# Kernel tuning notes

Hardware: AMD Instinct MI355X
Metric: run time of the kernel (lower is better)

## Reference

```python
import jax, jax.numpy as jnp
import numpy as np

N = 100000   # nodes
E = 1600000  # edges
D = 128      # input feature dim
H = 128      # hidden dim
L = 3        # gnn layers
G = 64       # graphs in batch
C = 2        # classes


def setup_inputs() -> dict:
    key = jax.random.key(0)
    ks = jax.random.split(key, 12)
    s = 0.05
    x = jax.random.normal(ks[0], (N, D), jnp.float32)
    edge_index = jax.random.randint(ks[1], (2, E), 0, N, dtype=jnp.int32)
    batch = jnp.sort(jax.random.randint(ks[2], (N,), 0, G, dtype=jnp.int32))
    return {
        "x": x,
        "edge_index": edge_index,
        "batch": batch,
        "W0": jax.random.normal(ks[3], (D, H), jnp.float32) * s,
        "b0": jnp.zeros((H,), jnp.float32),
        "Wg": jax.random.normal(ks[4], (L, H, H), jnp.float32) * s,
        "bg": jnp.zeros((L, H), jnp.float32),
        "Wc1": jax.random.normal(ks[5], (H, H), jnp.float32) * s,
        "bc1": jnp.zeros((H,), jnp.float32),
        "Wc2": jax.random.normal(ks[6], (H, C), jnp.float32) * s,
        "bc2": jnp.zeros((C,), jnp.float32),
    }


def reference(x, edge_index, batch, W0, b0, Wg, bg, Wc1, bc1, Wc2, bc2):
    # --- GCN normalization with self-loops (PyG gcn_norm) ---
    src, dst = edge_index[0], edge_index[1]
    loops = jnp.arange(N, dtype=src.dtype)
    src_f = jnp.concatenate([src, loops])  # [E+N] message sources (x_j)
    dst_f = jnp.concatenate([dst, loops])  # [E+N] aggregation targets
    deg = jax.ops.segment_sum(jnp.ones((E + N,), x.dtype), dst_f, num_segments=N)
    dinv = jnp.where(deg > 0, jax.lax.rsqrt(deg), 0.0)
    norm = (dinv[src_f] * dinv[dst_f])[:, None]  # [E+N, 1]

    # --- input linear + relu (dropout is identity in eval mode) ---
    h = jax.nn.relu(x @ W0 + b0)  # [N, H]

    # --- stacked GCNConv layers with residual + relu ---
    for l in range(L):
        xw = h @ Wg[l]  # [N, H]
        agg = jax.ops.segment_sum(xw[src_f] * norm, dst_f, num_segments=N) + bg[l]
        h = jax.nn.relu(h + agg)

    # --- global add pool over graphs ---
    pooled = jax.ops.segment_sum(h, batch, num_segments=G)  # [G, H]

    # --- classifier MLP + softmax ---
    z = jax.nn.relu(pooled @ Wc1 + bc1)
    return jax.nn.softmax(z @ Wc2 + bc2, axis=-1)  # [G, C]
```

## Files before the change

kernel.cpp:

```cpp
#include <hip/hip_runtime.h>

#define NN 100000
#define NE 1600000
#define HD 128
#define NG 64
#define NL 3
#define NBK 391
#define NEB 391
#define CAP 4608
#define NRB 6250
#define FP4_SCALE 8.0f
#define FP4_INV   0.125f

typedef __attribute__((ext_vector_type(8))) short bf16x8;
typedef __attribute__((ext_vector_type(4))) float f32x4;
typedef __attribute__((ext_vector_type(2))) float f32x2;
union U4 { uint4 u; bf16x8 b; };


__device__ __forceinline__ unsigned f2bf(float f) {
    unsigned u = __float_as_uint(f);
    return (u + 0x7FFFu + ((u >> 16) & 1u)) >> 16;
}
__device__ __forceinline__ float bf_lo(unsigned w) { return __uint_as_float(w << 16); }
__device__ __forceinline__ float bf_hi(unsigned w) { return __uint_as_float(w & 0xFFFF0000u); }
__device__ __forceinline__ unsigned cvt_pk_bf16(float lo, float hi) {
    unsigned r;
    asm("v_cvt_pk_bf16_f32 %0, %1, %2" : "=v"(r) : "v"(lo), "v"(hi));
    return r;
}


__global__ __launch_bounds__(256) void k_wconv(const float* __restrict__ W0,
                                               const float* __restrict__ Wg,
                                               unsigned* __restrict__ Wb) {
    int gid = blockIdx.x * 256 + threadIdx.x;
    for (int i = gid; i < 4 * 8192; i += 32 * 256) {
        int m = i >> 13;
        int r = i & 8191;
        int col = r & 127;
        int p = r >> 7;
        int k0, k1;
        if (m == 0) { k0 = 2 * p; k1 = 2 * p + 1; }
        else        { k0 = p;     k1 = p + 64;    }
        const float* Ws = (m == 0) ? W0 : (Wg + (m - 1) * 16384);
        float w0 = Ws[k0 * 128 + col];
        float w1 = Ws[k1 * 128 + col];
        Wb[m * 8192 + col * 64 + (((2 * p) ^ ((col & 7) << 3)) >> 1)] = (f2bf(w1) << 16) | f2bf(w0);
    }
}


__global__ __launch_bounds__(256) void k_bscatter(const int* __restrict__ src, const int* __restrict__ dst,
                                                  int* __restrict__ gcur, unsigned* __restrict__ pairs) {
    __shared__ int cnt[NBK];
    __shared__ int bse[NBK];
    __shared__ int rnk[NBK];
    for (int i = threadIdx.x; i < NBK; i += 256) { cnt[i] = 0; rnk[i] = 0; }
    __syncthreads();
    int base = blockIdx.x * 4096;
    int d[16];
#pragma unroll
    for (int j = 0; j < 16; j++) {
        int e = base + j * 256 + threadIdx.x;
        d[j] = (e < NE) ? dst[e] : -1;
        if (d[j] >= 0) atomicAdd(&cnt[((unsigned)d[j]) >> 8], 1);
    }
    __syncthreads();
    for (int i = threadIdx.x; i < NBK; i += 256) {
        int c = cnt[i];
        bse[i] = c ? atomicAdd(&gcur[i], c) : 0;
    }
    __syncthreads();
#pragma unroll
    for (int j = 0; j < 16; j++) {
        int e = base + j * 256 + threadIdx.x;
        if (e < NE) {
            int b = ((unsigned)d[j]) >> 8;
            int r = atomicAdd(&rnk[b], 1);
            int pos = bse[b] + r;
            if (pos < CAP)
                pairs[(size_t)b * CAP + pos] = (unsigned)src[e] | (((unsigned)d[j] & 255u) << 17);
        }
    }
}

__global__ __launch_bounds__(256) void k_bfill(const unsigned* __restrict__ pairs,
                                               const int* __restrict__ gcur,
                                               int* __restrict__ row_ptr, int* __restrict__ degA,
                                               float* __restrict__ dinv, unsigned* __restrict__ csr) {
    __shared__ int cnt[256];
    __shared__ int sm[256];
    __shared__ int cur[256];
    int t = threadIdx.x, k = blockIdx.x;
    int base = k * CAP;
    int ne = min(gcur[k], CAP);
    cnt[t] = 0;
    __syncthreads();
    for (int e = t; e < ne; e += 256) atomicAdd(&cnt[pairs[base + e] >> 17], 1);
    __syncthreads();
    int v = cnt[t];
    sm[t] = v;
    __syncthreads();
    for (int off = 1; off < 256; off <<= 1) {
        int add = (t >= off) ? sm[t - off] : 0;
        __syncthreads();
        sm[t] += add;
        __syncthreads();
    }
    int excl = base + sm[t] - v;
    int node = (k << 8) + t;
    if (node < NN) {
        row_ptr[node] = excl;
        degA[node] = v;
        dinv[node] = rsqrtf((float)(v + 1));
    }
    cur[t] = excl;
    __syncthreads();
    for (int e = t; e < ne; e += 256) {
        unsigned p = pairs[base + e];
        int pos = atomicAdd(&cur[p >> 17], 1);
        csr[pos] = (p & 0x1FFFFu) << 6;
    }
}


template <int MODE>
__global__ __launch_bounds__(256) void k_mgemm(
    const float* __restrict__ Xf, const unsigned* __restrict__ Xb,
    const unsigned* __restrict__ Wb, const float* __restrict__ bias,
    const float* __restrict__ dinv, unsigned* __restrict__ Out) {
    __shared__ unsigned short Bt[128 * 128];
    {
        const uint4* s4 = (const uint4*)Wb;
        uint4* d4 = (uint4*)Bt;
        for (int i = threadIdx.x; i < 2048; i += 256) d4[i] = s4[i];
    }
    __syncthreads();

    int lane = threadIdx.x & 63;
    int l15 = lane & 15, q = lane >> 4;
    int rb = blockIdx.x * 4 + (threadIdx.x >> 6);
    if (rb >= NRB) return;
    int r0 = rb * 16;

    U4 a[4];
    if (MODE == 0) {
        const float* xrow = Xf + (size_t)(r0 + l15) * 128 + q * 8;
#pragma unroll
        for (int kk = 0; kk < 4; kk++) {
            float4 f0 = *(const float4*)(xrow + kk * 32);
            float4 f1 = *(const float4*)(xrow + kk * 32 + 4);
            a[kk].u.x = (f2bf(f0.y) << 16) | f2bf(f0.x);
            a[kk].u.y = (f2bf(f0.w) << 16) | f2bf(f0.z);
            a[kk].u.z = (f2bf(f1.y) << 16) | f2bf(f1.x);
            a[kk].u.w = (f2bf(f1.w) << 16) | f2bf(f1.z);
        }
    } else {
        const unsigned* xrow = Xb + (size_t)(r0 + l15) * 64 + q * 4;
#pragma unroll
        for (int kk = 0; kk < 4; kk++) a[kk].u = *(const uint4*)(xrow + kk * 16);
    }

    f32x4 acc[8];
#pragma unroll
    for (int ct = 0; ct < 8; ct++) acc[ct] = (f32x4){0.f, 0.f, 0.f, 0.f};
#pragma unroll
    for (int kk = 0; kk < 4; kk++) {
#pragma unroll
        for (int ct = 0; ct < 8; ct++) {
            int col = ct * 16 + l15;
            int off = col * 128 + ((kk * 32 + q * 8) ^ ((col & 7) << 3));
            U4 b;
            b.u = *(const uint4*)&Bt[off];
            acc[ct] = __builtin_amdgcn_mfma_f32_16x16x32_bf16(a[kk].b, b.b, acc[ct], 0, 0, 0);
        }
    }

    if (MODE == 0) {
        float bv[8];
#pragma unroll
        for (int ct = 0; ct < 8; ct++) bv[ct] = bias[ct * 16 + l15];
#pragma unroll
        for (int r = 0; r < 4; r++) {
            int row = r0 + q * 4 + r;
#pragma unroll
            for (int ct = 0; ct < 4; ct++) {
                float lo = fmaxf(acc[ct][r] + bv[ct], 0.f);
                float hi = fmaxf(acc[ct + 4][r] + bv[ct + 4], 0.f);
                Out[(size_t)row * 64 + ct * 16 + l15] = cvt_pk_bf16(lo, hi);
            }
        }
    } else {
#pragma unroll
        for (int r = 0; r < 4; r++) {
            int row = r0 + q * 4 + r;
            float sc = dinv[row] * FP4_SCALE;
            unsigned dw = __builtin_amdgcn_cvt_scalef32_pk_fp4_f32(0u, acc[0][r] * sc, acc[4][r] * sc, 1.0f, 0);
            dw = __builtin_amdgcn_cvt_scalef32_pk_fp4_f32(dw, acc[2][r] * sc, acc[6][r] * sc, 1.0f, 1);
            dw = __builtin_amdgcn_cvt_scalef32_pk_fp4_f32(dw, acc[1][r] * sc, acc[5][r] * sc, 1.0f, 2);
            dw = __builtin_amdgcn_cvt_scalef32_pk_fp4_f32(dw, acc[3][r] * sc, acc[7][r] * sc, 1.0f, 3);
            Out[(size_t)row * 16 + l15] = dw;
        }
    }
}


__global__ __launch_bounds__(256) void k_aggregate(const unsigned char* __restrict__ xb,
                                                   unsigned* __restrict__ hb,
                                                   const int* __restrict__ row_ptr,
                                                   const int* __restrict__ degA,
                                                   const unsigned* __restrict__ csr,
                                                   const float* __restrict__ dinv,
                                                   const float* __restrict__ bg) {
    int wave = threadIdx.x >> 6;
    int lane = threadIdx.x & 63;
    int q = lane >> 4;
    int l16 = lane & 15;
    int sub = l16 >> 3;
    int l8 = l16 & 7;
    int node = blockIdx.x * 16 + wave * 4 + q;
    unsigned e = (unsigned)row_ptr[node];
    unsigned e1 = e + (unsigned)degA[node];
    unsigned loff = (unsigned)l8 * 8u;

    f32x2 p0 = {0.f, 0.f}, p1 = {0.f, 0.f}, p2 = {0.f, 0.f}, p3 = {0.f, 0.f};
    f32x2 q0 = {0.f, 0.f}, q1 = {0.f, 0.f}, q2 = {0.f, 0.f}, q3 = {0.f, 0.f};

#define ACC8(V) \
    p0 += __builtin_amdgcn_cvt_scalef32_pk_f32_fp4((V).x, 1.0f, 0); \
    p1 += __builtin_amdgcn_cvt_scalef32_pk_f32_fp4((V).x, 1.0f, 1); \
    p2 += __builtin_amdgcn_cvt_scalef32_pk_f32_fp4((V).x, 1.0f, 2); \
    p3 += __builtin_amdgcn_cvt_scalef32_pk_f32_fp4((V).x, 1.0f, 3); \
    q0 += __builtin_amdgcn_cvt_scalef32_pk_f32_fp4((V).y, 1.0f, 0); \
    q1 += __builtin_amdgcn_cvt_scalef32_pk_f32_fp4((V).y, 1.0f, 1); \
    q2 += __builtin_amdgcn_cvt_scalef32_pk_f32_fp4((V).y, 1.0f, 2); \
    q3 += __builtin_amdgcn_cvt_scalef32_pk_f32_fp4((V).y, 1.0f, 3);

    for (; e + 7 < e1; e += 8) {
        unsigned o0 = csr[e + sub];
        unsigned o1 = csr[e + 2 + sub];
        unsigned o2 = csr[e + 4 + sub];
        unsigned o3 = csr[e + 6 + sub];
        uint2 v0 = *(const uint2*)(xb + (o0 + loff));
        uint2 v1 = *(const uint2*)(xb + (o1 + loff));
        uint2 v2 = *(const uint2*)(xb + (o2 + loff));
        uint2 v3 = *(const uint2*)(xb + (o3 + loff));
        ACC8(v0); ACC8(v1); ACC8(v2); ACC8(v3);
    }
    if (e + 3 < e1) {
        unsigned o0 = csr[e + sub];
        unsigned o1 = csr[e + 2 + sub];
        uint2 v0 = *(const uint2*)(xb + (o0 + loff));
        uint2 v1 = *(const uint2*)(xb + (o1 + loff));
        ACC8(v0); ACC8(v1);
        e += 4;
    }
    if (e + 1 < e1) {
        unsigned o = csr[e + sub];
        uint2 v = *(const uint2*)(xb + (o + loff));
        ACC8(v);
        e += 2;
    }
    if (e + (unsigned)sub < e1) {
        unsigned o = csr[e + sub];
        uint2 v = *(const uint2*)(xb + (o + loff));
        ACC8(v);
    }
#undef ACC8

    f32x2 s0 = sub ? q0 : p0;
    f32x2 s1 = sub ? q1 : p1;
    f32x2 s2 = sub ? q2 : p2;
    f32x2 s3 = sub ? q3 : p3;
    f32x2 t0 = sub ? p0 : q0;
    f32x2 t1 = sub ? p1 : q1;
    f32x2 t2 = sub ? p2 : q2;
    f32x2 t3 = sub ? p3 : q3;
    s0.x += __shfl_xor(t0.x, 8); s0.y += __shfl_xor(t0.y, 8);
    s1.x += __shfl_xor(t1.x, 8); s1.y += __shfl_xor(t1.y, 8);
    s2.x += __shfl_xor(t2.x, 8); s2.y += __shfl_xor(t2.y, 8);
    s3.x += __shfl_xor(t3.x, 8); s3.y += __shfl_xor(t3.y, 8);

    int j_e = 2 * l8 + sub;

    unsigned ovd = *(const unsigned*)(xb + (((unsigned)node << 6) + (unsigned)j_e * 4u));
    s0 += __builtin_amdgcn_cvt_scalef32_pk_f32_fp4(ovd, 1.0f, 0);
    s1 += __builtin_amdgcn_cvt_scalef32_pk_f32_fp4(ovd, 1.0f, 1);
    s2 += __builtin_amdgcn_cvt_scalef32_pk_f32_fp4(ovd, 1.0f, 2);
    s3 += __builtin_amdgcn_cvt_scalef32_pk_f32_fp4(ovd, 1.0f, 3);

    float di2 = dinv[node] * FP4_INV;
    float a[8] = {s0.x, s0.y, s1.x, s1.y, s2.x, s2.y, s3.x, s3.y};
    size_t hbase = (size_t)node * 64;
    unsigned hv0 = hb[hbase + j_e];
    unsigned hv1 = hb[hbase + j_e + 32];
    unsigned hv2 = hb[hbase + j_e + 16];
    unsigned hv3 = hb[hbase + j_e + 48];
    float hh[8] = {bf_lo(hv0), bf_hi(hv0), bf_lo(hv1), bf_hi(hv1),
                   bf_lo(hv2), bf_hi(hv2), bf_lo(hv3), bf_hi(hv3)};
    float gg[8] = {bg[j_e], bg[j_e + 64], bg[j_e + 32], bg[j_e + 96],
                   bg[j_e + 16], bg[j_e + 80], bg[j_e + 48], bg[j_e + 112]};
    float r[8];
#pragma unroll
    for (int i = 0; i < 8; i++) r[i] = fmaxf(hh[i] + di2 * a[i] + gg[i], 0.f);
    hb[hbase + j_e]      = cvt_pk_bf16(r[0], r[1]);
    hb[hbase + j_e + 32] = cvt_pk_bf16(r[2], r[3]);
    hb[hbase + j_e + 16] = cvt_pk_bf16(r[4], r[5]);
    hb[hbase + j_e + 48] = cvt_pk_bf16(r[6], r[7]);
}


__global__ void k_bounds(const int* __restrict__ batch, int* __restrict__ start) {
    int i = blockIdx.x * blockDim.x + threadIdx.x;
    if (i >= NN) return;
    int b = batch[i];
    int prev = (i == 0) ? -1 : batch[i - 1];
    for (int g = prev + 1; g <= b; g++) start[g] = i;
    if (i == NN - 1) {
        for (int g = b + 1; g <= NG; g++) start[g] = NN;
    }
}

__global__ __launch_bounds__(128) void k_pool(const unsigned* __restrict__ hb,
                                              const int* __restrict__ start,
                                              float* __restrict__ pooled) {
    int g = blockIdx.x >> 4;
    int c = blockIdx.x & 15;
    int s = start[g], e = start[g + 1];
    int len = e - s;
    if (len <= 0) return;
    int chunk = (len + 15) >> 4;
    int r0 = s + c * chunk;
    int r1 = min(e, r0 + chunk);
    if (r0 >= r1) return;
    int jj = threadIdx.x & 63;
    int half = threadIdx.x >> 6;
    float ax = 0.f, ay = 0.f;
    for (int r = r0 + half; r < r1; r += 2) {
        unsigned v = hb[(size_t)r * 64 + jj];
        ax += bf_lo(v);
        ay += bf_hi(v);
    }
    atomicAdd(&pooled[g * 128 + jj], ax);
    atomicAdd(&pooled[g * 128 + jj + 64], ay);
}


__global__ __launch_bounds__(128) void k_classify(const float* __restrict__ pooled,
                                                  const float* __restrict__ Wc1,
                                                  const float* __restrict__ bc1,
                                                  const float* __restrict__ Wc2,
                                                  const float* __restrict__ bc2,
                                                  float* __restrict__ out) {
    __shared__ float p[128];
    __shared__ float r0s[128];
    __shared__ float r1s[128];
    int g = blockIdx.x;
    int j = threadIdx.x;
    p[j] = pooled[g * 128 + j];
    __syncthreads();
    float acc = bc1[j];
#pragma unroll 4
    for (int k = 0; k < 128; k++) acc = fmaf(p[k], Wc1[k * 128 + j], acc);
    float z = fmaxf(acc, 0.f);
    r0s[j] = z * Wc2[j * 2 + 0];
    r1s[j] = z * Wc2[j * 2 + 1];
    __syncthreads();
    for (int st = 64; st > 0; st >>= 1) {
        if (j < st) { r0s[j] += r0s[j + st]; r1s[j] += r1s[j + st]; }
        __syncthreads();
    }
    if (j == 0) {
        float l0 = r0s[0] + bc2[0];
        float l1 = r1s[0] + bc2[1];
        float m = fmaxf(l0, l1);
        float e0 = expf(l0 - m), e1 = expf(l1 - m);
        float inv = 1.f / (e0 + e1);
        out[g * 2 + 0] = e0 * inv;
        out[g * 2 + 1] = e1 * inv;
    }
}


extern "C" void kernel_launch(void* const* d_in, const int* in_sizes, int n_in,
                              void* d_out, int out_size, void* d_ws, size_t ws_size,
                              hipStream_t stream) {
    (void)in_sizes; (void)n_in; (void)out_size;

    const float* x     = (const float*)d_in[0];
    const int*   ei    = (const int*)d_in[1];
    const int*   batch = (const int*)d_in[2];
    const float* W0    = (const float*)d_in[3];
    const float* b0    = (const float*)d_in[4];
    const float* Wg    = (const float*)d_in[5];
    const float* bg    = (const float*)d_in[6];
    const float* Wc1   = (const float*)d_in[7];
    const float* bc1   = (const float*)d_in[8];
    const float* Wc2   = (const float*)d_in[9];
    const float* bc2   = (const float*)d_in[10];
    float* out = (float*)d_out;

    const int* srcp = ei;
    const int* dstp = ei + NE;

    char* w = (char*)d_ws;
    auto alloc = [&](size_t bytes) {
        char* p = w;
        w += (bytes + 255) & ~(size_t)255;
        return p;
    };
    unsigned* hb      = (unsigned*)alloc((size_t)NN * 64 * 4);
    unsigned* xws4    = (unsigned*)alloc((size_t)NN * 16 * 4);
    float*    dinv    = (float*)alloc((size_t)NN * 4);
    int*      row_ptr = (int*)alloc((size_t)NN * 4);
    int*      degA    = (int*)alloc((size_t)NN * 4);
    unsigned* csr     = (unsigned*)alloc((size_t)NBK * CAP * 4);
    unsigned* pairs   = (unsigned*)alloc((size_t)NBK * CAP * 4);
    int*      gcur    = (int*)alloc((size_t)NBK * 4);
    unsigned* Wb      = (unsigned*)alloc((size_t)4 * 8192 * 4);
    int*      start   = (int*)alloc((NG + 1) * 4);
    float*    pooled  = (float*)alloc((size_t)NG * HD * 4);
    if ((size_t)(w - (char*)d_ws) > ws_size) return;

    hipMemsetAsync(gcur, 0, NBK * 4, stream);
    hipMemsetAsync(pooled, 0, NG * HD * 4, stream);

    k_wconv<<<32, 256, 0, stream>>>(W0, Wg, Wb);
    k_bscatter<<<NEB, 256, 0, stream>>>(srcp, dstp, gcur, pairs);
    k_bfill<<<NBK, 256, 0, stream>>>(pairs, gcur, row_ptr, degA, dinv, csr);

    int gb = (NRB + 3) / 4;
    k_mgemm<0><<<gb, 256, 0, stream>>>(x, nullptr, Wb, b0, nullptr, hb);
    for (int l = 0; l < NL; l++) {
        k_mgemm<1><<<gb, 256, 0, stream>>>(nullptr, hb, Wb + (size_t)(l + 1) * 8192, nullptr, dinv, xws4);
        k_aggregate<<<NRB, 256, 0, stream>>>((const unsigned char*)xws4, hb, row_ptr, degA, csr, dinv, bg + l * HD);
    }
    k_bounds<<<(NN + 255) / 256, 256, 0, stream>>>(batch, start);
    k_pool<<<NG * 16, 128, 0, stream>>>(hb, start, pooled);
    k_classify<<<NG, 128, 0, stream>>>(pooled, Wc1, bc1, Wc2, bc2, out);
}
```

Baseline: 231.1 us.

## Split fp4 features into two column planes and aggregate per plane

The fp4 message buffer is stored as two planes of 32 bytes per node instead of one 64-byte row, and aggregation runs as two passes, each gathering one plane. Each pass touches a 3.2 MB working set, so the random gathers are more likely to hit in L2 or the last-level cache. The cost is twice as many aggregate launches, re-reading the CSR indices in each pass, and half the lanes idling in the epilogue. Separately, the weight conversion, edge bucketing and graph-bounds kernels are merged into one launch to cut launch overhead.

```diff
diff --git a/kernel.cpp b/kernel.cpp
--- a/kernel.cpp
+++ b/kernel.cpp
@@ -31,59 +31,74 @@
 }
 
 
-__global__ __launch_bounds__(256) void k_wconv(const float* __restrict__ W0,
-                                               const float* __restrict__ Wg,
-                                               unsigned* __restrict__ Wb) {
-    int gid = blockIdx.x * 256 + threadIdx.x;
-    for (int i = gid; i < 4 * 8192; i += 32 * 256) {
-        int m = i >> 13;
-        int r = i & 8191;
-        int col = r & 127;
-        int p = r >> 7;
-        int k0, k1;
-        if (m == 0) { k0 = 2 * p; k1 = 2 * p + 1; }
-        else        { k0 = p;     k1 = p + 64;    }
-        const float* Ws = (m == 0) ? W0 : (Wg + (m - 1) * 16384);
-        float w0 = Ws[k0 * 128 + col];
-        float w1 = Ws[k1 * 128 + col];
-        Wb[m * 8192 + col * 64 + (((2 * p) ^ ((col & 7) << 3)) >> 1)] = (f2bf(w1) << 16) | f2bf(w0);
-    }
-}
-
-
-__global__ __launch_bounds__(256) void k_bscatter(const int* __restrict__ src, const int* __restrict__ dst,
-                                                  int* __restrict__ gcur, unsigned* __restrict__ pairs) {
-    __shared__ int cnt[NBK];
-    __shared__ int bse[NBK];
-    __shared__ int rnk[NBK];
-    for (int i = threadIdx.x; i < NBK; i += 256) { cnt[i] = 0; rnk[i] = 0; }
-    __syncthreads();
-    int base = blockIdx.x * 4096;
-    int d[16];
-#pragma unroll
-    for (int j = 0; j < 16; j++) {
-        int e = base + j * 256 + threadIdx.x;
-        d[j] = (e < NE) ? dst[e] : -1;
-        if (d[j] >= 0) atomicAdd(&cnt[((unsigned)d[j]) >> 8], 1);
-    }
-    __syncthreads();
-    for (int i = threadIdx.x; i < NBK; i += 256) {
-        int c = cnt[i];
-        bse[i] = c ? atomicAdd(&gcur[i], c) : 0;
-    }
-    __syncthreads();
-#pragma unroll
-    for (int j = 0; j < 16; j++) {
-        int e = base + j * 256 + threadIdx.x;
-        if (e < NE) {
-            int b = ((unsigned)d[j]) >> 8;
-            int r = atomicAdd(&rnk[b], 1);
-            int pos = bse[b] + r;
-            if (pos < CAP)
-                pairs[(size_t)b * CAP + pos] = (unsigned)src[e] | (((unsigned)d[j] & 255u) << 17);
-        }
-    }
-}
+__global__ __launch_bounds__(256) void k_pre(const float* __restrict__ W0,
+                                             const float* __restrict__ Wg,
+                                             unsigned* __restrict__ Wb,
+                                             const int* __restrict__ src,
+                                             const int* __restrict__ dst,
+                                             int* __restrict__ gcur,
+                                             unsigned* __restrict__ pairs,
+                                             const int* __restrict__ batch,
+                                             int* __restrict__ start) {
+    int blk = blockIdx.x;
+    if (blk < 32) {
+        int gid = blk * 256 + threadIdx.x;
+        for (int i = gid; i < 4 * 8192; i += 32 * 256) {
+            int m = i >> 13;
+            int r = i & 8191;
+            int col = r & 127;
+            int p = r >> 7;
+            int k0, k1;
+            if (m == 0) { k0 = 2 * p; k1 = 2 * p + 1; }
+            else        { k0 = p;     k1 = p + 64;    }
+            const float* Ws = (m == 0) ? W0 : (Wg + (m - 1) * 16384);
+            float w0 = Ws[k0 * 128 + col];
+            float w1 = Ws[k1 * 128 + col];
+            Wb[m * 8192 + col * 64 + (((2 * p) ^ ((col & 7) << 3)) >> 1)] = (f2bf(w1) << 16) | f2bf(w0);
+        }
+    } else if (blk < 32 + NEB) {
+        __shared__ int cnt[NBK];
+        __shared__ int bse[NBK];
+        __shared__ int rnk[NBK];
+        for (int i = threadIdx.x; i < NBK; i += 256) { cnt[i] = 0; rnk[i] = 0; }
+        __syncthreads();
+        int base = (blk - 32) * 4096;
+        int d[16];
+#pragma unroll
+        for (int j = 0; j < 16; j++) {
+            int e = base + j * 256 + threadIdx.x;
+            d[j] = (e < NE) ? dst[e] : -1;
+            if (d[j] >= 0) atomicAdd(&cnt[((unsigned)d[j]) >> 8], 1);
+        }
+        __syncthreads();
+        for (int i = threadIdx.x; i < NBK; i += 256) {
+            int c = cnt[i];
+            bse[i] = c ? atomicAdd(&gcur[i], c) : 0;
+        }
+        __syncthreads();
+#pragma unroll
+        for (int j = 0; j < 16; j++) {
+            int e = base + j * 256 + threadIdx.x;
+            if (e < NE) {
+                int b = ((unsigned)d[j]) >> 8;
+                int r = atomicAdd(&rnk[b], 1);
+                int pos = bse[b] + r;
+                if (pos < CAP)
+                    pairs[(size_t)b * CAP + pos] = (unsigned)src[e] | (((unsigned)d[j] & 255u) << 17);
+            }
+        }
+    } else {
+        int i = (blk - 32 - NEB) * 256 + threadIdx.x;
+        if (i >= NN) return;
+        int b = batch[i];
+        int prev = (i == 0) ? -1 : batch[i - 1];
+        for (int g = prev + 1; g <= b; g++) start[g] = i;
+        if (i == NN - 1) {
+            for (int g = b + 1; g <= NG; g++) start[g] = NN;
+        }
+    }
+}
+
 
 __global__ __launch_bounds__(256) void k_bfill(const unsigned* __restrict__ pairs,
                                                const int* __restrict__ gcur,
@@ -120,7 +135,7 @@
     for (int e = t; e < ne; e += 256) {
         unsigned p = pairs[base + e];
         int pos = atomicAdd(&cur[p >> 17], 1);
-        csr[pos] = (p & 0x1FFFFu) << 6;
+        csr[pos] = (p & 0x1FFFFu) << 5;
     }
 }
 
@@ -192,6 +207,7 @@
             }
         }
     } else {
+        size_t pbase = (l15 < 8) ? (size_t)l15 : ((size_t)NN * 8 + (l15 - 8));
 #pragma unroll
         for (int r = 0; r < 4; r++) {
             int row = r0 + q * 4 + r;
@@ -200,29 +216,31 @@
             dw = __builtin_amdgcn_cvt_scalef32_pk_fp4_f32(dw, acc[2][r] * sc, acc[6][r] * sc, 1.0f, 1);
             dw = __builtin_amdgcn_cvt_scalef32_pk_fp4_f32(dw, acc[1][r] * sc, acc[5][r] * sc, 1.0f, 2);
             dw = __builtin_amdgcn_cvt_scalef32_pk_fp4_f32(dw, acc[3][r] * sc, acc[7][r] * sc, 1.0f, 3);
-            Out[(size_t)row * 16 + l15] = dw;
-        }
-    }
-}
-
-
-__global__ __launch_bounds__(256) void k_aggregate(const unsigned char* __restrict__ xb,
-                                                   unsigned* __restrict__ hb,
-                                                   const int* __restrict__ row_ptr,
-                                                   const int* __restrict__ degA,
-                                                   const unsigned* __restrict__ csr,
-                                                   const float* __restrict__ dinv,
-                                                   const float* __restrict__ bg) {
+            Out[pbase + (size_t)row * 8] = dw;
+        }
+    }
+}
+
+
+template <int P>
+__global__ __launch_bounds__(256) void k_aggpass(const unsigned char* __restrict__ xb,
+                                                 unsigned* __restrict__ hb,
+                                                 const int* __restrict__ row_ptr,
+                                                 const int* __restrict__ degA,
+                                                 const unsigned* __restrict__ csr,
+                                                 const float* __restrict__ dinv,
+                                                 const float* __restrict__ bg) {
     int wave = threadIdx.x >> 6;
     int lane = threadIdx.x & 63;
     int q = lane >> 4;
     int l16 = lane & 15;
-    int sub = l16 >> 3;
-    int l8 = l16 & 7;
+    int slot = l16 >> 2;
+    int l4 = l16 & 3;
     int node = blockIdx.x * 16 + wave * 4 + q;
     unsigned e = (unsigned)row_ptr[node];
     unsigned e1 = e + (unsigned)degA[node];
-    unsigned loff = (unsigned)l8 * 8u;
+    const unsigned char* plane = xb + (size_t)P * NN * 32;
+    unsigned loff = (unsigned)l4 * 8u;
 
     f32x2 p0 = {0.f, 0.f}, p1 = {0.f, 0.f}, p2 = {0.f, 0.f}, p3 = {0.f, 0.f};
     f32x2 q0 = {0.f, 0.f}, q1 = {0.f, 0.f}, q2 = {0.f, 0.f}, q3 = {0.f, 0.f};
@@ -238,53 +256,52 @@
     q3 += __builtin_amdgcn_cvt_scalef32_pk_f32_fp4((V).y, 1.0f, 3);
 
     for (; e + 7 < e1; e += 8) {
-        unsigned o0 = csr[e + sub];
-        unsigned o1 = csr[e + 2 + sub];
-        unsigned o2 = csr[e + 4 + sub];
-        unsigned o3 = csr[e + 6 + sub];
-        uint2 v0 = *(const uint2*)(xb + (o0 + loff));
-        uint2 v1 = *(const uint2*)(xb + (o1 + loff));
-        uint2 v2 = *(const uint2*)(xb + (o2 + loff));
-        uint2 v3 = *(const uint2*)(xb + (o3 + loff));
-        ACC8(v0); ACC8(v1); ACC8(v2); ACC8(v3);
-    }
-    if (e + 3 < e1) {
-        unsigned o0 = csr[e + sub];
-        unsigned o1 = csr[e + 2 + sub];
-        uint2 v0 = *(const uint2*)(xb + (o0 + loff));
-        uint2 v1 = *(const uint2*)(xb + (o1 + loff));
+        unsigned o0 = csr[e + slot];
+        unsigned o1 = csr[e + 4 + slot];
+        uint2 v0 = *(const uint2*)(plane + (o0 + loff));
+        uint2 v1 = *(const uint2*)(plane + (o1 + loff));
         ACC8(v0); ACC8(v1);
-        e += 4;
-    }
-    if (e + 1 < e1) {
-        unsigned o = csr[e + sub];
-        uint2 v = *(const uint2*)(xb + (o + loff));
+    }
+    if (e + (unsigned)slot < e1) {
+        unsigned o = csr[e + slot];
+        uint2 v = *(const uint2*)(plane + (o + loff));
         ACC8(v);
-        e += 2;
-    }
-    if (e + (unsigned)sub < e1) {
-        unsigned o = csr[e + sub];
-        uint2 v = *(const uint2*)(xb + (o + loff));
+    }
+    if (e + 4 + (unsigned)slot < e1) {
+        unsigned o = csr[e + 4 + slot];
+        uint2 v = *(const uint2*)(plane + (o + loff));
         ACC8(v);
     }
 #undef ACC8
 
-    f32x2 s0 = sub ? q0 : p0;
-    f32x2 s1 = sub ? q1 : p1;
-    f32x2 s2 = sub ? q2 : p2;
-    f32x2 s3 = sub ? q3 : p3;
-    f32x2 t0 = sub ? p0 : q0;
-    f32x2 t1 = sub ? p1 : q1;
-    f32x2 t2 = sub ? p2 : q2;
-    f32x2 t3 = sub ? p3 : q3;
-    s0.x += __shfl_xor(t0.x, 8); s0.y += __shfl_xor(t0.y, 8);
-    s1.x += __shfl_xor(t1.x, 8); s1.y += __shfl_xor(t1.y, 8);
-    s2.x += __shfl_xor(t2.x, 8); s2.y += __shfl_xor(t2.y, 8);
-    s3.x += __shfl_xor(t3.x, 8); s3.y += __shfl_xor(t3.y, 8);
-
-    int j_e = 2 * l8 + sub;
-
-    unsigned ovd = *(const unsigned*)(xb + (((unsigned)node << 6) + (unsigned)j_e * 4u));
+    p0.x += __shfl_xor(p0.x, 8); p0.y += __shfl_xor(p0.y, 8);
+    p1.x += __shfl_xor(p1.x, 8); p1.y += __shfl_xor(p1.y, 8);
+    p2.x += __shfl_xor(p2.x, 8); p2.y += __shfl_xor(p2.y, 8);
+    p3.x += __shfl_xor(p3.x, 8); p3.y += __shfl_xor(p3.y, 8);
+    q0.x += __shfl_xor(q0.x, 8); q0.y += __shfl_xor(q0.y, 8);
+    q1.x += __shfl_xor(q1.x, 8); q1.y += __shfl_xor(q1.y, 8);
+    q2.x += __shfl_xor(q2.x, 8); q2.y += __shfl_xor(q2.y, 8);
+    q3.x += __shfl_xor(q3.x, 8); q3.y += __shfl_xor(q3.y, 8);
+
+    int keep = slot & 1;
+    f32x2 s0 = keep ? q0 : p0;
+    f32x2 s1 = keep ? q1 : p1;
+    f32x2 s2 = keep ? q2 : p2;
+    f32x2 s3 = keep ? q3 : p3;
+    f32x2 t0 = keep ? p0 : q0;
+    f32x2 t1 = keep ? p1 : q1;
+    f32x2 t2 = keep ? p2 : q2;
+    f32x2 t3 = keep ? p3 : q3;
+    s0.x += __shfl_xor(t0.x, 4); s0.y += __shfl_xor(t0.y, 4);
+    s1.x += __shfl_xor(t1.x, 4); s1.y += __shfl_xor(t1.y, 4);
+    s2.x += __shfl_xor(t2.x, 4); s2.y += __shfl_xor(t2.y, 4);
+    s3.x += __shfl_xor(t3.x, 4); s3.y += __shfl_xor(t3.y, 4);
+
+    if (l16 >= 8) return;
+
+    int j_e = P * 8 + 2 * l4 + keep;
+
+    unsigned ovd = *(const unsigned*)(plane + ((unsigned)node * 32u) + (unsigned)(j_e & 7) * 4u);
     s0 += __builtin_amdgcn_cvt_scalef32_pk_f32_fp4(ovd, 1.0f, 0);
     s1 += __builtin_amdgcn_cvt_scalef32_pk_f32_fp4(ovd, 1.0f, 1);
     s2 += __builtin_amdgcn_cvt_scalef32_pk_f32_fp4(ovd, 1.0f, 2);
@@ -310,17 +327,6 @@
     hb[hbase + j_e + 48] = cvt_pk_bf16(r[6], r[7]);
 }
 
-
-__global__ void k_bounds(const int* __restrict__ batch, int* __restrict__ start) {
-    int i = blockIdx.x * blockDim.x + threadIdx.x;
-    if (i >= NN) return;
-    int b = batch[i];
-    int prev = (i == 0) ? -1 : batch[i - 1];
-    for (int g = prev + 1; g <= b; g++) start[g] = i;
-    if (i == NN - 1) {
-        for (int g = b + 1; g <= NG; g++) start[g] = NN;
-    }
-}
 
 __global__ __launch_bounds__(128) void k_pool(const unsigned* __restrict__ hb,
                                               const int* __restrict__ start,
@@ -426,17 +432,16 @@
     hipMemsetAsync(gcur, 0, NBK * 4, stream);
     hipMemsetAsync(pooled, 0, NG * HD * 4, stream);
 
-    k_wconv<<<32, 256, 0, stream>>>(W0, Wg, Wb);
-    k_bscatter<<<NEB, 256, 0, stream>>>(srcp, dstp, gcur, pairs);
+    k_pre<<<32 + NEB + 391, 256, 0, stream>>>(W0, Wg, Wb, srcp, dstp, gcur, pairs, batch, start);
     k_bfill<<<NBK, 256, 0, stream>>>(pairs, gcur, row_ptr, degA, dinv, csr);
 
     int gb = (NRB + 3) / 4;
     k_mgemm<0><<<gb, 256, 0, stream>>>(x, nullptr, Wb, b0, nullptr, hb);
     for (int l = 0; l < NL; l++) {
         k_mgemm<1><<<gb, 256, 0, stream>>>(nullptr, hb, Wb + (size_t)(l + 1) * 8192, nullptr, dinv, xws4);
-        k_aggregate<<<NRB, 256, 0, stream>>>((const unsigned char*)xws4, hb, row_ptr, degA, csr, dinv, bg + l * HD);
-    }
-    k_bounds<<<(NN + 255) / 256, 256, 0, stream>>>(batch, start);
+        k_aggpass<0><<<NRB, 256, 0, stream>>>((const unsigned char*)xws4, hb, row_ptr, degA, csr, dinv, bg + l * HD);
+        k_aggpass<1><<<NRB, 256, 0, stream>>>((const unsigned char*)xws4, hb, row_ptr, degA, csr, dinv, bg + l * HD);
+    }
     k_pool<<<NG * 16, 128, 0, stream>>>(hb, start, pooled);
     k_classify<<<NG, 128, 0, stream>>>(pooled, Wc1, bc1, Wc2, bc2, out);
 }
```

New measurement: 293.8 us. 27.2% more time.
